# Performance work log

Hardware: AMD Instinct MI355X
Metric: run time of the kernel (lower is better)

## Reference

```python
import jax, jax.numpy as jnp
import numpy as np

N, M, FIN, K, OUT, E = 8, 49152, 64, 6, 64, 393216


def setup_inputs() -> dict:
    key = jax.random.key(0)
    k1, k2, k3, k4, k5, k6 = jax.random.split(key, 6)
    x = jax.random.normal(k1, (N, M, FIN), jnp.float32)
    rows = jax.random.randint(k2, (E,), 0, M, jnp.int32)
    cols = jax.random.randint(k3, (E,), 0, M, jnp.int32)
    vals = jax.random.normal(k4, (E,), jnp.float32) * 0.1  # scaled-Laplacian values
    stdv = 1.0 / np.sqrt(OUT)
    weight = jax.random.uniform(k5, (FIN * K, OUT), jnp.float32, -stdv, stdv)
    bias = jax.random.uniform(k6, (OUT,), jnp.float32, -stdv, stdv)
    return {"x": x, "rows": rows, "cols": cols, "vals": vals,
            "weight": weight, "bias": bias}


def reference(x, rows, cols, vals, weight, bias):
    # x: [N, M, Fin]; L sparse [M, M] in COO (rows, cols, vals)
    n, m, fin = x.shape
    # x0: [M, Fin*N] as in torch permute(1,2,0).view(M, Fin*N)
    x0 = jnp.transpose(x, (1, 2, 0)).reshape(m, fin * n)

    def spmm(X):  # L @ X via gather + segment-sum scatter
        return jax.ops.segment_sum(vals[:, None] * X[cols], rows, num_segments=m)

    xs = [x0]
    if K > 1:
        x1 = spmm(x0)
        xs.append(x1)
        for _ in range(2, K):
            x2 = 2.0 * spmm(x1) - x0
            xs.append(x2)
            x0, x1 = x1, x2

    # stack -> [K, M, Fin, N]; torch then permutes to [N, M, Fin, K] and
    # flattens to (N*M, Fin*K) with Fin outer, K inner: weight row idx = f*K + k
    T = jnp.stack(xs, 0).reshape(K, m, fin, n)
    Wr = weight.reshape(fin, K, OUT)
    out = jnp.einsum('kmfn,fko->nmo', T, Wr) + bias  # [N, M, OUT]
    return jax.nn.elu(out)
```

## Files before the change

### kernel.cpp

```cpp
#include <hip/hip_runtime.h>
#include <hip/hip_bf16.h>
#include <math.h>

#define N_    8
#define M_    49152
#define FIN_  64
#define K_    6
#define OUT_  64
#define E_    393216
#define ROW_  512

typedef __attribute__((ext_vector_type(8))) short bf16x8;
typedef __attribute__((ext_vector_type(4))) float f32x4;

static __device__ __forceinline__ unsigned short f2bf(float f) {
    unsigned u = __float_as_uint(f);
    u += 0x7fff + ((u >> 16) & 1);
    return (unsigned short)(u >> 16);
}
static __device__ __forceinline__ float bfl(unsigned u) { return __uint_as_float(u << 16); }
static __device__ __forceinline__ float bfh(unsigned u) { return __uint_as_float(u & 0xffff0000u); }


__global__ void count_kernel(const int* __restrict__ rows, int* __restrict__ cnt) {
    int e = blockIdx.x * blockDim.x + threadIdx.x;
    if (e < E_) atomicAdd(&cnt[rows[e]], 1);
}

__global__ __launch_bounds__(1024) void scanA_kernel(const int* __restrict__ cnt,
                                                     int* __restrict__ lscan,
                                                     int* __restrict__ bsum) {
    __shared__ int wsum[16];
    int b = blockIdx.x, t = threadIdx.x, lane = t & 63, wid = t >> 6;
    int v = cnt[b * 1024 + t];
    int s = v;
    #pragma unroll
    for (int off = 1; off < 64; off <<= 1) {
        int y = __shfl_up(s, off, 64);
        if (lane >= off) s += y;
    }
    if (lane == 63) wsum[wid] = s;
    __syncthreads();
    if (t == 0) {
        int run = 0;
        #pragma unroll
        for (int i = 0; i < 16; ++i) { int c = wsum[i]; wsum[i] = run; run += c; }
        bsum[b] = run;
    }
    __syncthreads();
    lscan[b * 1024 + t] = wsum[wid] + s - v;
}

__global__ void scanB_kernel(const int* __restrict__ bsum, int* __restrict__ boffs,
                             int* __restrict__ rowptr) {
    int t = threadIdx.x;
    int v = (t < 48) ? bsum[t] : 0;
    int s = v;
    #pragma unroll
    for (int off = 1; off < 64; off <<= 1) {
        int y = __shfl_up(s, off, 64);
        if (t >= off) s += y;
    }
    if (t < 48) boffs[t] = s - v;
    if (t == 0) rowptr[M_] = E_;
}

__global__ __launch_bounds__(1024) void scanC_kernel(int* __restrict__ rowptr,
                                                     const int* __restrict__ boffs,
                                                     int* __restrict__ cntfill) {
    int b = blockIdx.x, t = threadIdx.x;
    int val = rowptr[b * 1024 + t] + boffs[b];
    rowptr[b * 1024 + t]  = val;
    cntfill[b * 1024 + t] = val;
}

__global__ void fill_kernel(const int* __restrict__ rows, const int* __restrict__ cols,
                            const float* __restrict__ vals, int* __restrict__ fillpos,
                            int* __restrict__ ecol, float* __restrict__ evalv,
                            int* __restrict__ eidx) {
    int e = blockIdx.x * blockDim.x + threadIdx.x;
    if (e < E_) {
        int r = rows[e];
        int p = atomicAdd(&fillpos[r], 1);
        ecol[p]  = cols[e];
        evalv[p] = vals[e];
        eidx[p]  = e;
    }
}

__global__ void sort_kernel(const int* __restrict__ rowptr, int* __restrict__ ecol,
                            float* __restrict__ evalv, int* __restrict__ eidx) {
    int m = blockIdx.x * blockDim.x + threadIdx.x;
    if (m >= M_) return;
    int s = rowptr[m], e = rowptr[m + 1];
    for (int i = s + 1; i < e; ++i) {
        int ki = eidx[i]; int kc = ecol[i]; float kv = evalv[i];
        int j = i - 1;
        while (j >= s && eidx[j] > ki) {
            eidx[j + 1] = eidx[j]; ecol[j + 1] = ecol[j]; evalv[j + 1] = evalv[j];
            --j;
        }
        eidx[j + 1] = ki; ecol[j + 1] = kc; evalv[j + 1] = kv;
    }
}


__global__ void permute_count_kernel(const float* __restrict__ x, unsigned short* __restrict__ T0,
                                     const int* __restrict__ rows, int* __restrict__ cnt) {
    int idx = blockIdx.x * blockDim.x + threadIdx.x;
    int f4 = idx & 15, n = (idx >> 4) & 7, m = idx >> 7;
    float4 v = ((const float4*)x)[(size_t)(n * M_ + m) * 16 + f4];
    ushort4 o;
    o.x = f2bf(v.x); o.y = f2bf(v.y); o.z = f2bf(v.z); o.w = f2bf(v.w);
    *(ushort4*)(T0 + (size_t)m * ROW_ + n * 64 + f4 * 4) = o;
    if (idx < E_) atomicAdd(&cnt[rows[idx]], 1);
}

__global__ void fill_wprep_kernel(const int* __restrict__ rows, const int* __restrict__ cols,
                                  const float* __restrict__ vals, int* __restrict__ fillpos,
                                  int* __restrict__ ecol, float* __restrict__ evalv,
                                  int* __restrict__ eidx,
                                  const float* __restrict__ W, unsigned short* __restrict__ Wfrag) {
    int e = blockIdx.x * blockDim.x + threadIdx.x;
    if (e < E_) {
        int r = rows[e];
        int p = atomicAdd(&fillpos[r], 1);
        ecol[p]  = cols[e];
        evalv[p] = vals[e];
        eidx[p]  = e;
    }
    if (e < 24576) {
        int i = e & 7, l = (e >> 3) & 63, tile = (e >> 9) & 3, kk = e >> 11;
        int kcheb = kk >> 1;
        int f = (kk & 1) * 32 + (l >> 4) * 8 + i;
        int o = tile * 16 + (l & 15);
        Wfrag[e] = f2bf(W[(f * K_ + kcheb) * OUT_ + o]);
    }
}

static __device__ __forceinline__ void fma_u4(float* acc, float v, uint4 u) {
    acc[0] += v * bfl(u.x); acc[1] += v * bfh(u.x);
    acc[2] += v * bfl(u.y); acc[3] += v * bfh(u.y);
    acc[4] += v * bfl(u.z); acc[5] += v * bfh(u.z);
    acc[6] += v * bfl(u.w); acc[7] += v * bfh(u.w);
}

__global__ __launch_bounds__(256) void spmm_bf16_kernel(
        const unsigned short* __restrict__ cur, const unsigned short* __restrict__ prev,
        unsigned short* __restrict__ nxt,
        const int* __restrict__ rowptr, const int* __restrict__ ecol,
        const float* __restrict__ evalv, float alpha, float beta) {
    int t = threadIdx.x;
    int w = t >> 6, l = t & 63;
    int m = blockIdx.x * 4 + w;
    int s = rowptr[m], e = rowptr[m + 1];
    int cnt = e - s;
    int myc = 0; float myv = 0.f;
    if (l < cnt) { myc = ecol[s + l]; myv = evalv[s + l]; }
    uint4 p;
    if (beta != 0.f) p = *(const uint4*)(prev + (size_t)m * ROW_ + l * 8);

    float acc[8] = {0.f, 0.f, 0.f, 0.f, 0.f, 0.f, 0.f, 0.f};
    int lim = cnt < 64 ? cnt : 64;
    int i = 0;
    for (; i + 8 <= lim; i += 8) {
        int c0 = __shfl(myc, i),     c1 = __shfl(myc, i + 1);
        int c2 = __shfl(myc, i + 2), c3 = __shfl(myc, i + 3);
        int c4 = __shfl(myc, i + 4), c5 = __shfl(myc, i + 5);
        int c6 = __shfl(myc, i + 6), c7 = __shfl(myc, i + 7);
        uint4 u0 = *(const uint4*)(cur + (size_t)c0 * ROW_ + l * 8);
        uint4 u1 = *(const uint4*)(cur + (size_t)c1 * ROW_ + l * 8);
        uint4 u2 = *(const uint4*)(cur + (size_t)c2 * ROW_ + l * 8);
        uint4 u3 = *(const uint4*)(cur + (size_t)c3 * ROW_ + l * 8);
        uint4 u4 = *(const uint4*)(cur + (size_t)c4 * ROW_ + l * 8);
        uint4 u5 = *(const uint4*)(cur + (size_t)c5 * ROW_ + l * 8);
        uint4 u6 = *(const uint4*)(cur + (size_t)c6 * ROW_ + l * 8);
        uint4 u7 = *(const uint4*)(cur + (size_t)c7 * ROW_ + l * 8);
        fma_u4(acc, __shfl(myv, i),     u0); fma_u4(acc, __shfl(myv, i + 1), u1);
        fma_u4(acc, __shfl(myv, i + 2), u2); fma_u4(acc, __shfl(myv, i + 3), u3);
        fma_u4(acc, __shfl(myv, i + 4), u4); fma_u4(acc, __shfl(myv, i + 5), u5);
        fma_u4(acc, __shfl(myv, i + 6), u6); fma_u4(acc, __shfl(myv, i + 7), u7);
    }
    if (i + 4 <= lim) {
        int c0 = __shfl(myc, i),     c1 = __shfl(myc, i + 1);
        int c2 = __shfl(myc, i + 2), c3 = __shfl(myc, i + 3);
        uint4 u0 = *(const uint4*)(cur + (size_t)c0 * ROW_ + l * 8);
        uint4 u1 = *(const uint4*)(cur + (size_t)c1 * ROW_ + l * 8);
        uint4 u2 = *(const uint4*)(cur + (size_t)c2 * ROW_ + l * 8);
        uint4 u3 = *(const uint4*)(cur + (size_t)c3 * ROW_ + l * 8);
        fma_u4(acc, __shfl(myv, i),     u0); fma_u4(acc, __shfl(myv, i + 1), u1);
        fma_u4(acc, __shfl(myv, i + 2), u2); fma_u4(acc, __shfl(myv, i + 3), u3);
        i += 4;
    }
    if (i + 2 <= lim) {
        int c0 = __shfl(myc, i), c1 = __shfl(myc, i + 1);
        uint4 u0 = *(const uint4*)(cur + (size_t)c0 * ROW_ + l * 8);
        uint4 u1 = *(const uint4*)(cur + (size_t)c1 * ROW_ + l * 8);
        fma_u4(acc, __shfl(myv, i), u0); fma_u4(acc, __shfl(myv, i + 1), u1);
        i += 2;
    }
    if (i < lim) {
        int c0 = __shfl(myc, i);
        uint4 u0 = *(const uint4*)(cur + (size_t)c0 * ROW_ + l * 8);
        fma_u4(acc, __shfl(myv, i), u0);
    }
    for (int j = 64; j < cnt; ++j) {
        int c0 = ecol[s + j];
        float v0 = evalv[s + j];
        uint4 u0 = *(const uint4*)(cur + (size_t)c0 * ROW_ + l * 8);
        fma_u4(acc, v0, u0);
    }
    #pragma unroll
    for (int j = 0; j < 8; ++j) acc[j] *= alpha;
    if (beta != 0.f) {
        acc[0] += beta * bfl(p.x); acc[1] += beta * bfh(p.x);
        acc[2] += beta * bfl(p.y); acc[3] += beta * bfh(p.y);
        acc[4] += beta * bfl(p.z); acc[5] += beta * bfh(p.z);
        acc[6] += beta * bfl(p.w); acc[7] += beta * bfh(p.w);
    }
    uint4 o;
    o.x = (unsigned)f2bf(acc[0]) | ((unsigned)f2bf(acc[1]) << 16);
    o.y = (unsigned)f2bf(acc[2]) | ((unsigned)f2bf(acc[3]) << 16);
    o.z = (unsigned)f2bf(acc[4]) | ((unsigned)f2bf(acc[5]) << 16);
    o.w = (unsigned)f2bf(acc[6]) | ((unsigned)f2bf(acc[7]) << 16);
    *(uint4*)(nxt + (size_t)m * ROW_ + l * 8) = o;
}

static __device__ __forceinline__ void epilogue_tile(
        f32x4 acc, int tile, int rbase, int col, float b,
        float* __restrict__ outn) {
    int c = tile * 16 + col;
    #pragma unroll
    for (int v = 0; v < 4; ++v) {
        float r = acc[v] + b;
        r = r > 0.f ? r : (__expf(r) - 1.f);
        outn[(size_t)(rbase + v) * OUT_ + c] = r;
    }
}

__global__ __launch_bounds__(256) void combine_kernel(
        const unsigned short* __restrict__ Tbase,
        const unsigned short* __restrict__ Wfrag,
        const float* __restrict__ bias, float* __restrict__ out) {
    __shared__ unsigned short wlds[24576];
    int t = threadIdx.x;
    {
        const uint4* src = (const uint4*)Wfrag;
        uint4* dst = (uint4*)wlds;
        #pragma unroll
        for (int i = 0; i < 12; ++i)
            dst[t + 256 * i] = src[t + 256 * i];
    }
    __syncthreads();

    int w = t >> 6, l = t & 63;
    int rowhalf = w & 1, nhalf = w >> 1;
    int m0 = blockIdx.x * 32 + rowhalf * 16;
    int arow = m0 + (l & 15);
    const size_t MROW = (size_t)M_ * ROW_;
    size_t abase0 = (size_t)arow * ROW_ + (l >> 4) * 8;
    int rbase = m0 + (l >> 4) * 4;
    int col = l & 15;
    float b0 = bias[col], b1 = bias[16 + col], b2 = bias[32 + col], b3 = bias[48 + col];

    #pragma unroll
    for (int ni = 0; ni < 4; ++ni) {
        int n = nhalf * 4 + ni;
        size_t abase = abase0 + n * 64;
        bf16x8 a[12];
        #pragma unroll
        for (int kk = 0; kk < 12; ++kk)
            a[kk] = *(const bf16x8*)(Tbase + (size_t)(kk >> 1) * MROW + abase + (kk & 1) * 32);

        f32x4 acc0 = {0.f, 0.f, 0.f, 0.f};
        f32x4 acc1 = {0.f, 0.f, 0.f, 0.f};
        f32x4 acc2 = {0.f, 0.f, 0.f, 0.f};
        f32x4 acc3 = {0.f, 0.f, 0.f, 0.f};
        #pragma unroll
        for (int kk = 0; kk < 12; ++kk) {
            const unsigned short* wp = wlds + ((size_t)(kk * 4) * 64 + l) * 8;
            bf16x8 q0 = *(const bf16x8*)(wp);
            bf16x8 q1 = *(const bf16x8*)(wp + 512);
            bf16x8 q2 = *(const bf16x8*)(wp + 1024);
            bf16x8 q3 = *(const bf16x8*)(wp + 1536);
            acc0 = __builtin_amdgcn_mfma_f32_16x16x32_bf16(a[kk], q0, acc0, 0, 0, 0);
            acc1 = __builtin_amdgcn_mfma_f32_16x16x32_bf16(a[kk], q1, acc1, 0, 0, 0);
            acc2 = __builtin_amdgcn_mfma_f32_16x16x32_bf16(a[kk], q2, acc2, 0, 0, 0);
            acc3 = __builtin_amdgcn_mfma_f32_16x16x32_bf16(a[kk], q3, acc3, 0, 0, 0);
        }

        float* outn = out + (size_t)n * ((size_t)M_ * OUT_);
        epilogue_tile(acc0, 0, rbase, col, b0, outn);
        epilogue_tile(acc1, 1, rbase, col, b1, outn);
        epilogue_tile(acc2, 2, rbase, col, b2, outn);
        epilogue_tile(acc3, 3, rbase, col, b3, outn);
    }
}


__global__ void permute_kernel(const float* __restrict__ x, float* __restrict__ A) {
    int idx = blockIdx.x * blockDim.x + threadIdx.x;
    int f4 = idx & 15;
    int n  = (idx >> 4) & 7;
    int m  = idx >> 7;
    float4 v = ((const float4*)x)[(size_t)(n * M_ + m) * 16 + f4];
    ((float4*)A)[idx] = v;
}

__global__ __launch_bounds__(512) void step_kernel(
        const float* __restrict__ cur, float* __restrict__ nxt,
        const float* __restrict__ weight, const float* __restrict__ bias,
        const int* __restrict__ rowptr, const int* __restrict__ ecol,
        const float* __restrict__ evalv, float* __restrict__ out,
        int k, float alpha, float beta, int flags) {
    __shared__ float lds_x[ROW_];
    int m = blockIdx.x;
    int t = threadIdx.x;
    lds_x[t] = cur[(size_t)m * ROW_ + t];
    if (flags & 4) {
        float acc = 0.f;
        int s = rowptr[m], e = rowptr[m + 1];
        for (int i = s; i < e; ++i)
            acc += evalv[i] * cur[(size_t)ecol[i] * ROW_ + t];
        float prevv = (beta != 0.f) ? nxt[(size_t)m * ROW_ + t] : 0.f;
        nxt[(size_t)m * ROW_ + t] = alpha * acc + beta * prevv;
    }
    __syncthreads();
    int n = t >> 6, o = t & 63;
    const float4* lx4 = (const float4*)(lds_x + n * FIN_);
    float acc = 0.f;
    #pragma unroll
    for (int f4 = 0; f4 < 16; ++f4) {
        float4 xq = lx4[f4];
        int fb = f4 * 4;
        acc += xq.x * weight[((fb + 0) * K_ + k) * OUT_ + o];
        acc += xq.y * weight[((fb + 1) * K_ + k) * OUT_ + o];
        acc += xq.z * weight[((fb + 2) * K_ + k) * OUT_ + o];
        acc += xq.w * weight[((fb + 3) * K_ + k) * OUT_ + o];
    }
    size_t oidx = (size_t)n * (M_ * OUT_) + (size_t)m * OUT_ + o;
    float res = (flags & 1) ? acc : (out[oidx] + acc);
    if (flags & 2) {
        res += bias[o];
        res = (res > 0.f) ? res : (expf(res) - 1.f);
    }
    out[oidx] = res;
}


extern "C" void kernel_launch(void* const* d_in, const int* in_sizes, int n_in,
                              void* d_out, int out_size, void* d_ws, size_t ws_size,
                              hipStream_t stream) {
    (void)in_sizes; (void)n_in; (void)out_size;
    const float* x      = (const float*)d_in[0];
    const int*   rows   = (const int*)d_in[1];
    const int*   cols   = (const int*)d_in[2];
    const float* vals   = (const float*)d_in[3];
    const float* weight = (const float*)d_in[4];
    const float* bias   = (const float*)d_in[5];
    float* out = (float*)d_out;

    char* ws = (char*)d_ws;
    size_t off = 0;
    auto alloc = [&](size_t bytes) -> void* {
        void* p = ws + off;
        off += (bytes + 255) & ~(size_t)255;
        return p;
    };

    const size_t tbytes = (size_t)M_ * ROW_ * 2;
    const size_t need_new = 6 * (tbytes + 256) + (M_ + 1) * 4 + M_ * 4
                          + 3 * ((size_t)E_ * 4 + 256) + 24576 * 2 + 8192;

    if (ws_size >= need_new) {
        unsigned short* T[6];
        for (int i = 0; i < 6; ++i) T[i] = (unsigned short*)alloc(tbytes);
        int*   rowptr  = (int*)alloc((size_t)(M_ + 1) * 4);
        int*   fillpos = (int*)alloc((size_t)M_ * 4);
        int*   ecol    = (int*)alloc((size_t)E_ * 4);
        float* evalv   = (float*)alloc((size_t)E_ * 4);
        int*   eidx    = (int*)alloc((size_t)E_ * 4);
        unsigned short* Wfrag = (unsigned short*)alloc(24576 * 2);
        int*   bsum    = (int*)alloc(48 * 4);
        int*   boffs   = (int*)alloc(48 * 4);

        hipMemsetAsync(fillpos, 0, (size_t)M_ * 4, stream);
        permute_count_kernel<<<(M_ * N_ * 16) / 256, 256, 0, stream>>>(x, T[0], rows, fillpos);
        scanA_kernel<<<48, 1024, 0, stream>>>(fillpos, rowptr, bsum);
        scanB_kernel<<<1, 64, 0, stream>>>(bsum, boffs, rowptr);
        scanC_kernel<<<48, 1024, 0, stream>>>(rowptr, boffs, fillpos);
        fill_wprep_kernel<<<E_ / 256, 256, 0, stream>>>(rows, cols, vals, fillpos,
                                                        ecol, evalv, eidx, weight, Wfrag);
        sort_kernel<<<M_ / 256, 256, 0, stream>>>(rowptr, ecol, evalv, eidx);

        spmm_bf16_kernel<<<M_ / 4, 256, 0, stream>>>(T[0], T[0], T[1], rowptr, ecol, evalv, 1.f, 0.f);
        spmm_bf16_kernel<<<M_ / 4, 256, 0, stream>>>(T[1], T[0], T[2], rowptr, ecol, evalv, 2.f, -1.f);
        spmm_bf16_kernel<<<M_ / 4, 256, 0, stream>>>(T[2], T[1], T[3], rowptr, ecol, evalv, 2.f, -1.f);
        spmm_bf16_kernel<<<M_ / 4, 256, 0, stream>>>(T[3], T[2], T[4], rowptr, ecol, evalv, 2.f, -1.f);
        spmm_bf16_kernel<<<M_ / 4, 256, 0, stream>>>(T[4], T[3], T[5], rowptr, ecol, evalv, 2.f, -1.f);

        combine_kernel<<<M_ / 32, 256, 0, stream>>>(T[0], Wfrag, bias, out);
    } else {
        float* A       = (float*)alloc((size_t)M_ * ROW_ * 4);
        float* B       = (float*)alloc((size_t)M_ * ROW_ * 4);
        int*   rowptr  = (int*)alloc((size_t)(M_ + 1) * 4);
        int*   fillpos = (int*)alloc((size_t)M_ * 4);
        int*   ecol    = (int*)alloc((size_t)E_ * 4);
        float* evalv   = (float*)alloc((size_t)E_ * 4);
        int*   eidx    = (int*)alloc((size_t)E_ * 4);
        int*   bsum    = (int*)alloc(48 * 4);
        int*   boffs   = (int*)alloc(48 * 4);

        permute_kernel<<<(M_ * N_ * 16) / 256, 256, 0, stream>>>(x, A);
        hipMemsetAsync(fillpos, 0, (size_t)M_ * 4, stream);
        count_kernel<<<E_ / 256, 256, 0, stream>>>(rows, fillpos);
        scanA_kernel<<<48, 1024, 0, stream>>>(fillpos, rowptr, bsum);
        scanB_kernel<<<1, 64, 0, stream>>>(bsum, boffs, rowptr);
        scanC_kernel<<<48, 1024, 0, stream>>>(rowptr, boffs, fillpos);
        fill_kernel<<<E_ / 256, 256, 0, stream>>>(rows, cols, vals, fillpos, ecol, evalv, eidx);
        sort_kernel<<<M_ / 256, 256, 0, stream>>>(rowptr, ecol, evalv, eidx);

        step_kernel<<<M_, 512, 0, stream>>>(A, B, weight, bias, rowptr, ecol, evalv, out, 0, 1.f, 0.f, 1 | 4);
        step_kernel<<<M_, 512, 0, stream>>>(B, A, weight, bias, rowptr, ecol, evalv, out, 1, 2.f, -1.f, 4);
        step_kernel<<<M_, 512, 0, stream>>>(A, B, weight, bias, rowptr, ecol, evalv, out, 2, 2.f, -1.f, 4);
        step_kernel<<<M_, 512, 0, stream>>>(B, A, weight, bias, rowptr, ecol, evalv, out, 3, 2.f, -1.f, 4);
        step_kernel<<<M_, 512, 0, stream>>>(A, B, weight, bias, rowptr, ecol, evalv, out, 4, 2.f, -1.f, 4);
        step_kernel<<<M_, 512, 0, stream>>>(B, B, weight, bias, rowptr, ecol, evalv, out, 5, 0.f, 0.f, 2);
    }
}
```

Measured before the change: 530.9 us.

## Hold weight fragments in registers per wave and sort edges by column

The combine kernel stops staging the weight matrix in LDS. Each wave now keeps the weight fragment for one 16-column output tile in registers and loops over both row tiles and all eight batches, so the block barrier and LDS reads go away. The trade-off is that every wave reloads the same A fragments from global memory, giving four times the A traffic, which the cache may or may not absorb. Separately, each row's edges are now sorted by (column, edge index) rather than edge index alone, which may improve gather locality in the SpMM steps but reorders the floating-point summation.

New measurement: 643.2 us. 21.2% more time.

```diff
diff --git a/kernel.cpp b/kernel.cpp
--- a/kernel.cpp
+++ b/kernel.cpp
@@ -94,9 +94,10 @@
     if (m >= M_) return;
     int s = rowptr[m], e = rowptr[m + 1];
     for (int i = s + 1; i < e; ++i) {
-        int ki = eidx[i]; int kc = ecol[i]; float kv = evalv[i];
+        int kc = ecol[i]; int ki = eidx[i]; float kv = evalv[i];
+        long long key = ((long long)kc << 20) | ki;
         int j = i - 1;
-        while (j >= s && eidx[j] > ki) {
+        while (j >= s && ((((long long)ecol[j]) << 20) | eidx[j]) > key) {
             eidx[j + 1] = eidx[j]; ecol[j + 1] = ecol[j]; evalv[j + 1] = evalv[j];
             --j;
         }
@@ -226,74 +227,49 @@
     *(uint4*)(nxt + (size_t)m * ROW_ + l * 8) = o;
 }
 
-static __device__ __forceinline__ void epilogue_tile(
-        f32x4 acc, int tile, int rbase, int col, float b,
-        float* __restrict__ outn) {
-    int c = tile * 16 + col;
-    #pragma unroll
-    for (int v = 0; v < 4; ++v) {
-        float r = acc[v] + b;
-        r = r > 0.f ? r : (__expf(r) - 1.f);
-        outn[(size_t)(rbase + v) * OUT_ + c] = r;
-    }
-}
-
 __global__ __launch_bounds__(256) void combine_kernel(
         const unsigned short* __restrict__ Tbase,
         const unsigned short* __restrict__ Wfrag,
         const float* __restrict__ bias, float* __restrict__ out) {
-    __shared__ unsigned short wlds[24576];
     int t = threadIdx.x;
-    {
-        const uint4* src = (const uint4*)Wfrag;
-        uint4* dst = (uint4*)wlds;
-        #pragma unroll
-        for (int i = 0; i < 12; ++i)
-            dst[t + 256 * i] = src[t + 256 * i];
-    }
-    __syncthreads();
-
-    int w = t >> 6, l = t & 63;
-    int rowhalf = w & 1, nhalf = w >> 1;
-    int m0 = blockIdx.x * 32 + rowhalf * 16;
-    int arow = m0 + (l & 15);
+    int tw = t >> 6, l = t & 63;
+
+    bf16x8 wreg[12];
+    #pragma unroll
+    for (int kk = 0; kk < 12; ++kk)
+        wreg[kk] = *(const bf16x8*)(Wfrag + ((size_t)(kk * 4 + tw) * 64 + l) * 8);
+
     const size_t MROW = (size_t)M_ * ROW_;
-    size_t abase0 = (size_t)arow * ROW_ + (l >> 4) * 8;
-    int rbase = m0 + (l >> 4) * 4;
-    int col = l & 15;
-    float b0 = bias[col], b1 = bias[16 + col], b2 = bias[32 + col], b3 = bias[48 + col];
-
-    #pragma unroll
-    for (int ni = 0; ni < 4; ++ni) {
-        int n = nhalf * 4 + ni;
-        size_t abase = abase0 + n * 64;
-        bf16x8 a[12];
-        #pragma unroll
-        for (int kk = 0; kk < 12; ++kk)
-            a[kk] = *(const bf16x8*)(Tbase + (size_t)(kk >> 1) * MROW + abase + (kk & 1) * 32);
-
-        f32x4 acc0 = {0.f, 0.f, 0.f, 0.f};
-        f32x4 acc1 = {0.f, 0.f, 0.f, 0.f};
-        f32x4 acc2 = {0.f, 0.f, 0.f, 0.f};
-        f32x4 acc3 = {0.f, 0.f, 0.f, 0.f};
-        #pragma unroll
-        for (int kk = 0; kk < 12; ++kk) {
-            const unsigned short* wp = wlds + ((size_t)(kk * 4) * 64 + l) * 8;
-            bf16x8 q0 = *(const bf16x8*)(wp);
-            bf16x8 q1 = *(const bf16x8*)(wp + 512);
-            bf16x8 q2 = *(const bf16x8*)(wp + 1024);
-            bf16x8 q3 = *(const bf16x8*)(wp + 1536);
-            acc0 = __builtin_amdgcn_mfma_f32_16x16x32_bf16(a[kk], q0, acc0, 0, 0, 0);
-            acc1 = __builtin_amdgcn_mfma_f32_16x16x32_bf16(a[kk], q1, acc1, 0, 0, 0);
-            acc2 = __builtin_amdgcn_mfma_f32_16x16x32_bf16(a[kk], q2, acc2, 0, 0, 0);
-            acc3 = __builtin_amdgcn_mfma_f32_16x16x32_bf16(a[kk], q3, acc3, 0, 0, 0);
+    int m0 = blockIdx.x * 32;
+    int col = tw * 16 + (l & 15);
+    float b = bias[col];
+
+    #pragma unroll
+    for (int rt = 0; rt < 2; ++rt) {
+        int arow = m0 + rt * 16 + (l & 15);
+        size_t abase0 = (size_t)arow * ROW_ + (l >> 4) * 8;
+        int rbase = m0 + rt * 16 + (l >> 4) * 4;
+        #pragma unroll 2
+        for (int n = 0; n < 8; ++n) {
+            size_t abase = abase0 + (size_t)n * 64;
+            bf16x8 a[12];
+            #pragma unroll
+            for (int kk = 0; kk < 12; ++kk)
+                a[kk] = *(const bf16x8*)(Tbase + (size_t)(kk >> 1) * MROW + abase + (kk & 1) * 32);
+
+            f32x4 acc = {0.f, 0.f, 0.f, 0.f};
+            #pragma unroll
+            for (int kk = 0; kk < 12; ++kk)
+                acc = __builtin_amdgcn_mfma_f32_16x16x32_bf16(a[kk], wreg[kk], acc, 0, 0, 0);
+
+            float* outn = out + (size_t)n * ((size_t)M_ * OUT_);
+            #pragma unroll
+            for (int v = 0; v < 4; ++v) {
+                float r = acc[v] + b;
+                r = r > 0.f ? r : (__expf(r) - 1.f);
+                outn[(size_t)(rbase + v) * OUT_ + col] = r;
+            }
         }
-
-        float* outn = out + (size_t)n * ((size_t)M_ * OUT_);
-        epilogue_tile(acc0, 0, rbase, col, b0, outn);
-        epilogue_tile(acc1, 1, rbase, col, b1, outn);
-        epilogue_tile(acc2, 2, rbase, col, b2, outn);
-        epilogue_tile(acc3, 3, rbase, col, b3, outn);
     }
 }
 
```
